# Kernel optimization log

Measured on AMD Instinct MI355X. Metric: run time of the kernel, lower is better.

## Reference

```python
import jax, jax.numpy as jnp
import numpy as np
from jax import lax

MAX_SCALE = 4
SCALES = [2 ** i for i in range(1, MAX_SCALE + 1)]  # [2,4,8,16]
EPS_K = 1e-7        # tf.keras.backend.epsilon()
BN_EPS = 1e-3       # keras BatchNormalization default epsilon


def sample_min_max_scaling(x):
    # per-sample min-max scaling over H, W, C
    mn = jnp.min(x, axis=(1, 2, 3), keepdims=True)
    mx = jnp.max(x, axis=(1, 2, 3), keepdims=True)
    return (x - mn) / (mx - mn + EPS_K)


def box_sum(x, r):
    # depthwise all-ones r x r conv, SAME padding (TF semantics)
    c = x.shape[-1]
    kernel = jnp.ones((r, r, 1, c), dtype=x.dtype)  # HWIO, depthwise
    return lax.conv_general_dilated(
        x, kernel, window_strides=(1, 1), padding='SAME',
        dimension_numbers=('NHWC', 'HWIO', 'NHWC'),
        feature_group_count=c)


def reference(x, gamma, beta, moving_mean, moving_var):
    x = sample_min_max_scaling(x)
    # multi-scale box-filter measures: [B,H,W,C,S]
    measures = jnp.stack([box_sum(x, r) for r in SCALES], axis=-1)
    # OLS slope of log(measure) vs log(scale) across the scale axis
    log_scales = jnp.log(jnp.asarray(SCALES, dtype=x.dtype))       # [S]
    log_measures = jnp.log(measures + EPS_K)                        # [B,H,W,C,S]
    mean_ls = jnp.mean(log_scales)
    mean_lm = jnp.mean(log_measures, axis=-1, keepdims=True)
    dls = log_scales - mean_ls                                      # [S]
    num = jnp.sum((log_measures - mean_lm) * dls, axis=-1)          # [B,H,W,C]
    den = jnp.sum(dls ** 2)
    alphas = num / den
    # BatchNormalization in inference mode (training=False)
    return (alphas - moving_mean) / jnp.sqrt(moving_var + BN_EPS) * gamma + beta


def setup_inputs() -> dict:
    key = jax.random.key(0)
    B, H, W, C = 16, 224, 224, 32
    x = jax.random.normal(key, (B, H, W, C), dtype=jnp.float32)
    return {
        'x': x,
        'gamma': jnp.ones((C,), jnp.float32),
        'beta': jnp.zeros((C,), jnp.float32),
        'moving_mean': jnp.zeros((C,), jnp.float32),
        'moving_var': jnp.ones((C,), jnp.float32),
    }
```

## Files before the change

### kernel.cpp

```cpp
#include <hip/hip_runtime.h>
#include <cstdint>

#define B_ 16
#define H_ 224
#define W_ 224
#define C_ 32
#define TS 32
#define RG 47
#define SR 48
#define SP 49

__device__ __forceinline__ unsigned int enc_f(float f) {
    unsigned int u = __float_as_uint(f);
    return (u & 0x80000000u) ? ~u : (u | 0x80000000u);
}
__device__ __forceinline__ float dec_f(unsigned int u) {
    u = (u & 0x80000000u) ? (u & 0x7FFFFFFFu) : ~u;
    return __uint_as_float(u);
}

__global__ void init_ws(unsigned int* __restrict__ ws) {
    int t = threadIdx.x;
    if (t < 16) ws[t] = 0xFFFFFFFFu;
    else if (t < 32) ws[t] = 0u;
}

__device__ __forceinline__ void blk_minmax(const float* __restrict__ x,
                                           float& mn, float& mx) {
    const int b = blockIdx.x;
    const int chunk = blockIdx.y;
    const int chunkElems = (H_ * W_ * C_) / 64;
    const float4* p = (const float4*)(x + (size_t)b * (H_ * W_ * C_) +
                                      (size_t)chunk * chunkElems);
    const int n4 = chunkElems / 4;
    mn = 3.4e38f; mx = -3.4e38f;
    for (int i = threadIdx.x; i < n4; i += 256) {
        float4 v = p[i];
        mn = fminf(mn, fminf(fminf(v.x, v.y), fminf(v.z, v.w)));
        mx = fmaxf(mx, fmaxf(fmaxf(v.x, v.y), fmaxf(v.z, v.w)));
    }
#pragma unroll
    for (int off = 32; off > 0; off >>= 1) {
        mn = fminf(mn, __shfl_down(mn, off));
        mx = fmaxf(mx, __shfl_down(mx, off));
    }
    __shared__ float smn[4], smx[4];
    const int lane = threadIdx.x & 63, wv = threadIdx.x >> 6;
    if (lane == 0) { smn[wv] = mn; smx[wv] = mx; }
    __syncthreads();
    mn = fminf(fminf(smn[0], smn[1]), fminf(smn[2], smn[3]));
    mx = fmaxf(fmaxf(smx[0], smx[1]), fmaxf(smx[2], smx[3]));
}

__global__ __launch_bounds__(256) void minmax_slots(const float* __restrict__ x,
                                                    float* __restrict__ wsf) {
    float mn, mx;
    blk_minmax(x, mn, mx);
    if (threadIdx.x == 0) {
        wsf[blockIdx.y * 16 + blockIdx.x] = mn;
        wsf[1024 + blockIdx.y * 16 + blockIdx.x] = mx;
    }
}

__global__ __launch_bounds__(256) void minmax_atomic(const float* __restrict__ x,
                                                     unsigned int* __restrict__ ws) {
    float mn, mx;
    blk_minmax(x, mn, mx);
    if (threadIdx.x == 0) {
        atomicMin(&ws[blockIdx.x], enc_f(mn));
        atomicMax(&ws[16 + blockIdx.x], enc_f(mx));
    }
}

template<int CTRL, int MASK>
__device__ __forceinline__ float dpp_add(float x) {
    int t = __builtin_amdgcn_update_dpp(0, (int)__float_as_uint(x),
                                        CTRL, MASK, 0xf, false);
    return x + __uint_as_float((unsigned)t);
}
template<int CTRL, int MASK>
__device__ __forceinline__ void dpp_step4(float4& v) {
    v.x = dpp_add<CTRL, MASK>(v.x);
    v.y = dpp_add<CTRL, MASK>(v.y);
    v.z = dpp_add<CTRL, MASK>(v.z);
    v.w = dpp_add<CTRL, MASK>(v.w);
}
__device__ __forceinline__ void hscan(float4& v) {
    dpp_step4<0x111, 0xf>(v);
    dpp_step4<0x112, 0xf>(v);
    dpp_step4<0x114, 0xf>(v);
    dpp_step4<0x118, 0xf>(v);
    dpp_step4<0x142, 0xa>(v);
    dpp_step4<0x143, 0xc>(v);
}

#define CL(a) (fmaxf((a), 0.0f) + 1e-7f)

#define BOXD(S, o, sc, bx) {                                             \
        float4 q00 = S[hl + (o)][wl + (o)];                              \
        float4 q01 = S[hl + (o)][wl + (o) + (sc)];                       \
        float4 q10 = S[hl + (o) + (sc)][wl + (o)];                       \
        float4 q11 = S[hl + (o) + (sc)][wl + (o) + (sc)];                \
        bx.x = q11.x - q01.x - q10.x + q00.x;                            \
        bx.y = q11.y - q01.y - q10.y + q00.y;                            \
        bx.z = q11.z - q01.z - q10.z + q00.z;                            \
        bx.w = q11.w - q01.w - q10.w + q00.w; }

#define BNPREP(qi, wq, oq) {                                             \
        const int ch0 = chbase + (qi) * 4;                               \
        const float4 g4  = *(const float4*)(gamma + ch0);                \
        const float4 be4 = *(const float4*)(beta  + ch0);                \
        const float4 mm4 = *(const float4*)(mmean + ch0);                \
        const float4 mv4 = *(const float4*)(mvar  + ch0);                \
        float t;                                                         \
        t = g4.x * rsqrtf(mv4.x + 1e-3f);                                \
        wq.x = 0.1f * t; oq.x = be4.x - mm4.x * t;                       \
        t = g4.y * rsqrtf(mv4.y + 1e-3f);                                \
        wq.y = 0.1f * t; oq.y = be4.y - mm4.y * t;                       \
        t = g4.z * rsqrtf(mv4.z + 1e-3f);                                \
        wq.z = 0.1f * t; oq.z = be4.z - mm4.z * t;                       \
        t = g4.w * rsqrtf(mv4.w + 1e-3f);                                \
        wq.w = 0.1f * t; oq.w = be4.w - mm4.w * t; }

#define LSSCOMP(comp, wq, oq, OUT) {                                     \
        const float a2 = CL(b2.comp),  a4 = CL(b4.comp);                 \
        const float a8 = CL(b8.comp),  a16 = CL(b16.comp);               \
        const float Lq = __log2f(a16 * a16 * a16 * a8)                   \
                       - __log2f(a2 * a2 * a2 * a4);                     \
        OUT = fmaf(Lq, wq.comp, oq.comp); }

#define DOQUAD(qi, wq, oq, o4) {                                         \
        const float4 (*S)[SP] = SAT[qi];                                 \
        float4 b2, b4, b8, b16;                                          \
        BOXD(S, 7, 2, b2);                                               \
        BOXD(S, 6, 4, b4);                                               \
        BOXD(S, 4, 8, b8);                                               \
        BOXD(S, 0, 16, b16);                                             \
        LSSCOMP(x, wq, oq, o4.x); LSSCOMP(y, wq, oq, o4.y);              \
        LSSCOMP(z, wq, oq, o4.z); LSSCOMP(w, wq, oq, o4.w); }

template<bool SLOTS>
__global__ __launch_bounds__(512, 4) void lss_kernel(
    const float* __restrict__ x,
    const float* __restrict__ gamma, const float* __restrict__ beta,
    const float* __restrict__ mmean, const float* __restrict__ mvar,
    const unsigned int* __restrict__ ws,
    float* __restrict__ out)
{
    __shared__ float4 SAT[2][SR][SP];

    const int bi = blockIdx.x;
    const int grp = bi >> 5, wi = bi & 31;
    const int tile = grp * 8 + (wi & 7);
    const int s  = (wi >> 3) & 1;
    const int qp = (wi >> 4) & 1;
    const int b = tile / 49;
    const int t2 = tile - b * 49;
    const int th0 = (t2 / 7) * TS;
    const int tw0 = (t2 % 7) * TS;
    const int tid = threadIdx.x;
    const int lane = tid & 63, wv = tid >> 6;
    const int chbase = s * 16 + qp * 8;

    float mn, mx;
    if (SLOTS) {
        const float* wsf = (const float*)ws;
        float vmn = wsf[lane * 16 + b];
        float vmx = wsf[1024 + lane * 16 + b];
#pragma unroll
        for (int off = 32; off > 0; off >>= 1) {
            vmn = fminf(vmn, __shfl_xor(vmn, off));
            vmx = fmaxf(vmx, __shfl_xor(vmx, off));
        }
        mn = vmn; mx = vmx;
    } else {
        mn = dec_f(ws[b]);
        mx = dec_f(ws[16 + b]);
    }
    const float inv = 1.0f / (mx - mn + 1e-7f);
    const float nmi = -mn * inv;

    const float* xb = x + (size_t)b * (H_ * W_ * C_);
    float* ob = out + (size_t)b * (H_ * W_ * C_);

#pragma unroll
    for (int p = 0; p < 6; ++p) {
        const int rr = wv + 8 * p;
        if (rr < RG) {
            const int gh = th0 - 7 + rr;
            const int gw = tw0 - 7 + lane;
            float4 q0 = make_float4(0.f, 0.f, 0.f, 0.f);
            float4 q1 = q0;
            if (lane < RG && gh >= 0 && gh < H_ && gw >= 0 && gw < W_) {
                const float4* p4 = (const float4*)(xb +
                    ((size_t)(gh * W_ + gw)) * C_ + chbase);
                q0 = p4[0]; q1 = p4[1];
                q0.x = fmaf(q0.x, inv, nmi); q0.y = fmaf(q0.y, inv, nmi);
                q0.z = fmaf(q0.z, inv, nmi); q0.w = fmaf(q0.w, inv, nmi);
                q1.x = fmaf(q1.x, inv, nmi); q1.y = fmaf(q1.y, inv, nmi);
                q1.z = fmaf(q1.z, inv, nmi); q1.w = fmaf(q1.w, inv, nmi);
            }
            hscan(q0); hscan(q1);
            if (lane < RG) {
                SAT[0][rr][lane + 1] = q0;
                SAT[1][rr][lane + 1] = q1;
            } else if (lane == 63) {
                const float4 z = make_float4(0.f, 0.f, 0.f, 0.f);
                SAT[0][rr][0] = z; SAT[1][rr][0] = z;
            }
        }
    }
    __syncthreads();

    {
        int q = -1, c = 0;
        if (tid < 192)      { q = 0; c = tid; }
        else if (tid < 384) { q = 1; c = tid - 192; }
        if (q >= 0) {
            float* col = (float*)&SAT[q][0][0] + c;
            float accv = 0.f;
#pragma unroll
            for (int r = 0; r < SR; ++r) {
                const float t = (r < RG) ? col[r * (SP * 4)] : 0.f;
                col[r * (SP * 4)] = accv;
                accv += t;
            }
        }
    }
    __syncthreads();

    {
        const int wl = tid & 31;
        const int hl0 = tid >> 5;
        float4 wq0, oq0, wq1, oq1;
        BNPREP(0, wq0, oq0);
        BNPREP(1, wq1, oq1);
#pragma unroll
        for (int pp = 0; pp < 2; ++pp) {
            const int hl = hl0 + pp * 16;
            float4 o0, o1;
            DOQUAD(0, wq0, oq0, o0);
            DOQUAD(1, wq1, oq1, o1);
            float* dst = ob + ((size_t)((th0 + hl) * W_ + (tw0 + wl))) * C_ + chbase;
            *(float4*)(dst + 0) = o0;
            *(float4*)(dst + 4) = o1;
        }
    }
}

extern "C" void kernel_launch(void* const* d_in, const int* in_sizes, int n_in,
                              void* d_out, int out_size, void* d_ws, size_t ws_size,
                              hipStream_t stream) {
    const float* x     = (const float*)d_in[0];
    const float* gamma = (const float*)d_in[1];
    const float* beta  = (const float*)d_in[2];
    const float* mmean = (const float*)d_in[3];
    const float* mvar  = (const float*)d_in[4];
    float* out = (float*)d_out;
    unsigned int* ws = (unsigned int*)d_ws;

    if (ws_size >= 8192) {
        hipLaunchKernelGGL(minmax_slots, dim3(16, 64), dim3(256), 0, stream,
                           x, (float*)ws);
        hipLaunchKernelGGL((lss_kernel<true>), dim3(98 * 32), dim3(512), 0, stream,
                           x, gamma, beta, mmean, mvar, ws, out);
    } else {
        hipLaunchKernelGGL(init_ws, dim3(1), dim3(64), 0, stream, ws);
        hipLaunchKernelGGL(minmax_atomic, dim3(16, 64), dim3(256), 0, stream, x, ws);
        hipLaunchKernelGGL((lss_kernel<false>), dim3(98 * 32), dim3(512), 0, stream,
                           x, gamma, beta, mmean, mvar, ws, out);
    }
}
```

Measured before the change: 261.7 us.

## Split channel work per block and share row-difference terms across output rows

Each block now handles 4 channels with 256 threads instead of 8 channels with 512 threads, so the block count doubles and shared memory per block halves. In the evaluation phase each thread computes four output rows that are 8 apart and reuses the horizontal SAT differences shared between overlapping boxes, which cuts LDS reads. It also combines the two log2 terms into one per side. The aim is fewer shared-memory reads and higher occupancy. The cost is more registers per thread and 16-byte instead of 32-byte global accesses per pixel.

Measured after the change: 270.3 us. 3.3% more time.

```diff
diff --git a/kernel.cpp b/kernel.cpp
--- a/kernel.cpp
+++ b/kernel.cpp
@@ -94,73 +94,41 @@
     dpp_step4<0x143, 0xc>(v);
 }
 
-#define CL(a) (fmaxf((a), 0.0f) + 1e-7f)
-
-#define BOXD(S, o, sc, bx) {                                             \
-        float4 q00 = S[hl + (o)][wl + (o)];                              \
-        float4 q01 = S[hl + (o)][wl + (o) + (sc)];                       \
-        float4 q10 = S[hl + (o) + (sc)][wl + (o)];                       \
-        float4 q11 = S[hl + (o) + (sc)][wl + (o) + (sc)];                \
-        bx.x = q11.x - q01.x - q10.x + q00.x;                            \
-        bx.y = q11.y - q01.y - q10.y + q00.y;                            \
-        bx.z = q11.z - q01.z - q10.z + q00.z;                            \
-        bx.w = q11.w - q01.w - q10.w + q00.w; }
-
-#define BNPREP(qi, wq, oq) {                                             \
-        const int ch0 = chbase + (qi) * 4;                               \
-        const float4 g4  = *(const float4*)(gamma + ch0);                \
-        const float4 be4 = *(const float4*)(beta  + ch0);                \
-        const float4 mm4 = *(const float4*)(mmean + ch0);                \
-        const float4 mv4 = *(const float4*)(mvar  + ch0);                \
-        float t;                                                         \
-        t = g4.x * rsqrtf(mv4.x + 1e-3f);                                \
-        wq.x = 0.1f * t; oq.x = be4.x - mm4.x * t;                       \
-        t = g4.y * rsqrtf(mv4.y + 1e-3f);                                \
-        wq.y = 0.1f * t; oq.y = be4.y - mm4.y * t;                       \
-        t = g4.z * rsqrtf(mv4.z + 1e-3f);                                \
-        wq.z = 0.1f * t; oq.z = be4.z - mm4.z * t;                       \
-        t = g4.w * rsqrtf(mv4.w + 1e-3f);                                \
-        wq.w = 0.1f * t; oq.w = be4.w - mm4.w * t; }
-
-#define LSSCOMP(comp, wq, oq, OUT) {                                     \
-        const float a2 = CL(b2.comp),  a4 = CL(b4.comp);                 \
-        const float a8 = CL(b8.comp),  a16 = CL(b16.comp);               \
-        const float Lq = __log2f(a16 * a16 * a16 * a8)                   \
-                       - __log2f(a2 * a2 * a2 * a4);                     \
-        OUT = fmaf(Lq, wq.comp, oq.comp); }
-
-#define DOQUAD(qi, wq, oq, o4) {                                         \
-        const float4 (*S)[SP] = SAT[qi];                                 \
-        float4 b2, b4, b8, b16;                                          \
-        BOXD(S, 7, 2, b2);                                               \
-        BOXD(S, 6, 4, b4);                                               \
-        BOXD(S, 4, 8, b8);                                               \
-        BOXD(S, 0, 16, b16);                                             \
-        LSSCOMP(x, wq, oq, o4.x); LSSCOMP(y, wq, oq, o4.y);              \
-        LSSCOMP(z, wq, oq, o4.z); LSSCOMP(w, wq, oq, o4.w); }
+__device__ __forceinline__ float4 f4sub(float4 a, float4 b) {
+    return make_float4(a.x - b.x, a.y - b.y, a.z - b.z, a.w - b.w);
+}
+__device__ __forceinline__ float4 f4mul(float4 a, float4 b) {
+    return make_float4(a.x * b.x, a.y * b.y, a.z * b.z, a.w * b.w);
+}
+__device__ __forceinline__ float4 f4cl(float4 a) {
+    return make_float4(fmaxf(a.x, 0.f) + 1e-7f, fmaxf(a.y, 0.f) + 1e-7f,
+                       fmaxf(a.z, 0.f) + 1e-7f, fmaxf(a.w, 0.f) + 1e-7f);
+}
+__device__ __forceinline__ float4 f4cube(float4 a) {
+    return f4mul(f4mul(a, a), a);
+}
 
 template<bool SLOTS>
-__global__ __launch_bounds__(512, 4) void lss_kernel(
+__global__ __launch_bounds__(256, 4) void lss_kernel(
     const float* __restrict__ x,
     const float* __restrict__ gamma, const float* __restrict__ beta,
     const float* __restrict__ mmean, const float* __restrict__ mvar,
     const unsigned int* __restrict__ ws,
     float* __restrict__ out)
 {
-    __shared__ float4 SAT[2][SR][SP];
+    __shared__ float4 SAT[SR][SP];
 
     const int bi = blockIdx.x;
-    const int grp = bi >> 5, wi = bi & 31;
+    const int grp = bi >> 6, wi = bi & 63;
     const int tile = grp * 8 + (wi & 7);
-    const int s  = (wi >> 3) & 1;
-    const int qp = (wi >> 4) & 1;
+    const int cq = (wi >> 3) & 7;
+    const int chbase = cq * 4;
     const int b = tile / 49;
     const int t2 = tile - b * 49;
     const int th0 = (t2 / 7) * TS;
     const int tw0 = (t2 % 7) * TS;
     const int tid = threadIdx.x;
     const int lane = tid & 63, wv = tid >> 6;
-    const int chbase = s * 16 + qp * 8;
 
     float mn, mx;
     if (SLOTS) {
@@ -184,67 +152,122 @@
     float* ob = out + (size_t)b * (H_ * W_ * C_);
 
 #pragma unroll
-    for (int p = 0; p < 6; ++p) {
-        const int rr = wv + 8 * p;
+    for (int p = 0; p < 12; ++p) {
+        const int rr = wv + 4 * p;
         if (rr < RG) {
             const int gh = th0 - 7 + rr;
             const int gw = tw0 - 7 + lane;
-            float4 q0 = make_float4(0.f, 0.f, 0.f, 0.f);
-            float4 q1 = q0;
+            float4 q = make_float4(0.f, 0.f, 0.f, 0.f);
             if (lane < RG && gh >= 0 && gh < H_ && gw >= 0 && gw < W_) {
-                const float4* p4 = (const float4*)(xb +
-                    ((size_t)(gh * W_ + gw)) * C_ + chbase);
-                q0 = p4[0]; q1 = p4[1];
-                q0.x = fmaf(q0.x, inv, nmi); q0.y = fmaf(q0.y, inv, nmi);
-                q0.z = fmaf(q0.z, inv, nmi); q0.w = fmaf(q0.w, inv, nmi);
-                q1.x = fmaf(q1.x, inv, nmi); q1.y = fmaf(q1.y, inv, nmi);
-                q1.z = fmaf(q1.z, inv, nmi); q1.w = fmaf(q1.w, inv, nmi);
+                q = *(const float4*)(xb + ((size_t)(gh * W_ + gw)) * C_ + chbase);
+                q.x = fmaf(q.x, inv, nmi); q.y = fmaf(q.y, inv, nmi);
+                q.z = fmaf(q.z, inv, nmi); q.w = fmaf(q.w, inv, nmi);
             }
-            hscan(q0); hscan(q1);
-            if (lane < RG) {
-                SAT[0][rr][lane + 1] = q0;
-                SAT[1][rr][lane + 1] = q1;
-            } else if (lane == 63) {
-                const float4 z = make_float4(0.f, 0.f, 0.f, 0.f);
-                SAT[0][rr][0] = z; SAT[1][rr][0] = z;
-            }
+            hscan(q);
+            if (lane < RG) SAT[rr][lane + 1] = q;
+            else if (lane == 63) SAT[rr][0] = make_float4(0.f, 0.f, 0.f, 0.f);
         }
     }
     __syncthreads();
 
+    if (tid < 192) {
+        float* col = (float*)&SAT[0][0] + tid;
+        float accv = 0.f;
+#pragma unroll
+        for (int r = 0; r < SR; ++r) {
+            const float t = (r < RG) ? col[r * (SP * 4)] : 0.f;
+            col[r * (SP * 4)] = accv;
+            accv += t;
+        }
+    }
+    __syncthreads();
+
     {
-        int q = -1, c = 0;
-        if (tid < 192)      { q = 0; c = tid; }
-        else if (tid < 384) { q = 1; c = tid - 192; }
-        if (q >= 0) {
-            float* col = (float*)&SAT[q][0][0] + c;
-            float accv = 0.f;
-#pragma unroll
-            for (int r = 0; r < SR; ++r) {
-                const float t = (r < RG) ? col[r * (SP * 4)] : 0.f;
-                col[r * (SP * 4)] = accv;
-                accv += t;
-            }
-        }
-    }
-    __syncthreads();
-
-    {
+        const int h = tid >> 5;
         const int wl = tid & 31;
-        const int hl0 = tid >> 5;
-        float4 wq0, oq0, wq1, oq1;
-        BNPREP(0, wq0, oq0);
-        BNPREP(1, wq1, oq1);
-#pragma unroll
-        for (int pp = 0; pp < 2; ++pp) {
-            const int hl = hl0 + pp * 16;
-            float4 o0, o1;
-            DOQUAD(0, wq0, oq0, o0);
-            DOQUAD(1, wq1, oq1, o1);
-            float* dst = ob + ((size_t)((th0 + hl) * W_ + (tw0 + wl))) * C_ + chbase;
-            *(float4*)(dst + 0) = o0;
-            *(float4*)(dst + 4) = o1;
-        }
+
+        float4 wq, oq;
+        {
+            const float4 g4  = *(const float4*)(gamma + chbase);
+            const float4 be4 = *(const float4*)(beta  + chbase);
+            const float4 mm4 = *(const float4*)(mmean + chbase);
+            const float4 mv4 = *(const float4*)(mvar  + chbase);
+            float t;
+            t = g4.x * rsqrtf(mv4.x + 1e-3f); wq.x = 0.1f * t; oq.x = be4.x - mm4.x * t;
+            t = g4.y * rsqrtf(mv4.y + 1e-3f); wq.y = 0.1f * t; oq.y = be4.y - mm4.y * t;
+            t = g4.z * rsqrtf(mv4.z + 1e-3f); wq.z = 0.1f * t; oq.z = be4.z - mm4.z * t;
+            t = g4.w * rsqrtf(mv4.w + 1e-3f); wq.w = 0.1f * t; oq.w = be4.w - mm4.w * t;
+        }
+
+        float4 num0, num1, num2, num3;
+        float4 den0, den1, den2, den3;
+
+        {
+            float4 e0 = f4sub(SAT[h     ][wl + 16], SAT[h     ][wl]);
+            float4 e1 = f4sub(SAT[h +  8][wl + 16], SAT[h +  8][wl]);
+            float4 e2 = f4sub(SAT[h + 16][wl + 16], SAT[h + 16][wl]);
+            float4 e3 = f4sub(SAT[h + 24][wl + 16], SAT[h + 24][wl]);
+            float4 e4 = f4sub(SAT[h + 32][wl + 16], SAT[h + 32][wl]);
+            float4 e5 = f4sub(SAT[h + 40][wl + 16], SAT[h + 40][wl]);
+            num0 = f4cube(f4cl(f4sub(e2, e0)));
+            num1 = f4cube(f4cl(f4sub(e3, e1)));
+            num2 = f4cube(f4cl(f4sub(e4, e2)));
+            num3 = f4cube(f4cl(f4sub(e5, e3)));
+        }
+        {
+            float4 e0 = f4sub(SAT[h +  4][wl + 12], SAT[h +  4][wl + 4]);
+            float4 e1 = f4sub(SAT[h + 12][wl + 12], SAT[h + 12][wl + 4]);
+            float4 e2 = f4sub(SAT[h + 20][wl + 12], SAT[h + 20][wl + 4]);
+            float4 e3 = f4sub(SAT[h + 28][wl + 12], SAT[h + 28][wl + 4]);
+            float4 e4 = f4sub(SAT[h + 36][wl + 12], SAT[h + 36][wl + 4]);
+            num0 = f4mul(num0, f4cl(f4sub(e1, e0)));
+            num1 = f4mul(num1, f4cl(f4sub(e2, e1)));
+            num2 = f4mul(num2, f4cl(f4sub(e3, e2)));
+            num3 = f4mul(num3, f4cl(f4sub(e4, e3)));
+        }
+        {
+            float4 t0, b0;
+            t0 = f4sub(SAT[h +  6][wl + 10], SAT[h +  6][wl + 6]);
+            b0 = f4sub(SAT[h + 10][wl + 10], SAT[h + 10][wl + 6]);
+            den0 = f4cl(f4sub(b0, t0));
+            t0 = f4sub(SAT[h + 14][wl + 10], SAT[h + 14][wl + 6]);
+            b0 = f4sub(SAT[h + 18][wl + 10], SAT[h + 18][wl + 6]);
+            den1 = f4cl(f4sub(b0, t0));
+            t0 = f4sub(SAT[h + 22][wl + 10], SAT[h + 22][wl + 6]);
+            b0 = f4sub(SAT[h + 26][wl + 10], SAT[h + 26][wl + 6]);
+            den2 = f4cl(f4sub(b0, t0));
+            t0 = f4sub(SAT[h + 30][wl + 10], SAT[h + 30][wl + 6]);
+            b0 = f4sub(SAT[h + 34][wl + 10], SAT[h + 34][wl + 6]);
+            den3 = f4cl(f4sub(b0, t0));
+        }
+        {
+            float4 t0, b0;
+            t0 = f4sub(SAT[h +  7][wl + 9], SAT[h +  7][wl + 7]);
+            b0 = f4sub(SAT[h +  9][wl + 9], SAT[h +  9][wl + 7]);
+            den0 = f4mul(den0, f4cube(f4cl(f4sub(b0, t0))));
+            t0 = f4sub(SAT[h + 15][wl + 9], SAT[h + 15][wl + 7]);
+            b0 = f4sub(SAT[h + 17][wl + 9], SAT[h + 17][wl + 7]);
+            den1 = f4mul(den1, f4cube(f4cl(f4sub(b0, t0))));
+            t0 = f4sub(SAT[h + 23][wl + 9], SAT[h + 23][wl + 7]);
+            b0 = f4sub(SAT[h + 25][wl + 9], SAT[h + 25][wl + 7]);
+            den2 = f4mul(den2, f4cube(f4cl(f4sub(b0, t0))));
+            t0 = f4sub(SAT[h + 31][wl + 9], SAT[h + 31][wl + 7]);
+            b0 = f4sub(SAT[h + 33][wl + 9], SAT[h + 33][wl + 7]);
+            den3 = f4mul(den3, f4cube(f4cl(f4sub(b0, t0))));
+        }
+#define FIN(NUM, DEN, ROW) {                                             \
+        float4 o4;                                                       \
+        o4.x = fmaf(__log2f(NUM.x) - __log2f(DEN.x), wq.x, oq.x);        \
+        o4.y = fmaf(__log2f(NUM.y) - __log2f(DEN.y), wq.y, oq.y);        \
+        o4.z = fmaf(__log2f(NUM.z) - __log2f(DEN.z), wq.z, oq.z);        \
+        o4.w = fmaf(__log2f(NUM.w) - __log2f(DEN.w), wq.w, oq.w);        \
+        *(float4*)(ob + ((size_t)((th0 + (ROW)) * W_ + (tw0 + wl))) * C_ \
+                   + chbase) = o4; }
+        FIN(num0, den0, h);
+        FIN(num1, den1, h + 8);
+        FIN(num2, den2, h + 16);
+        FIN(num3, den3, h + 24);
+#undef FIN
     }
 }
 
@@ -262,12 +285,12 @@
     if (ws_size >= 8192) {
         hipLaunchKernelGGL(minmax_slots, dim3(16, 64), dim3(256), 0, stream,
                            x, (float*)ws);
-        hipLaunchKernelGGL((lss_kernel<true>), dim3(98 * 32), dim3(512), 0, stream,
+        hipLaunchKernelGGL((lss_kernel<true>), dim3(98 * 64), dim3(256), 0, stream,
                            x, gamma, beta, mmean, mvar, ws, out);
     } else {
         hipLaunchKernelGGL(init_ws, dim3(1), dim3(64), 0, stream, ws);
         hipLaunchKernelGGL(minmax_atomic, dim3(16, 64), dim3(256), 0, stream, x, ws);
-        hipLaunchKernelGGL((lss_kernel<false>), dim3(98 * 32), dim3(512), 0, stream,
+        hipLaunchKernelGGL((lss_kernel<false>), dim3(98 * 64), dim3(256), 0, stream,
                            x, gamma, beta, mmean, mvar, ws, out);
     }
 }
```

## Split channel work to one float4 quad per block to halve LDS and raise occupancy

Applied to the files above, without the earlier changes.

Each block now handles 4 channels instead of 8, so the shared-memory summed-area table shrinks from two float4 planes to one (about 37 KB instead of 75 KB). The grid doubles and launch bounds request 8 blocks per CU instead of 4, aiming for more resident waves to hide memory and LDS latency. In exchange, each block loads its 47x47 halo per 4 channels, so halo reads and the per-tile prologue (min/max reduction, column scan) are duplicated across twice as many blocks. Global accesses become 16-byte per pixel instead of 32-byte, which lowers coalescing efficiency.

Result: no change. 261.7 us (+0.0%).

```diff
diff --git a/kernel.cpp b/kernel.cpp
--- a/kernel.cpp
+++ b/kernel.cpp
@@ -106,22 +106,6 @@
         bx.z = q11.z - q01.z - q10.z + q00.z;                            \
         bx.w = q11.w - q01.w - q10.w + q00.w; }
 
-#define BNPREP(qi, wq, oq) {                                             \
-        const int ch0 = chbase + (qi) * 4;                               \
-        const float4 g4  = *(const float4*)(gamma + ch0);                \
-        const float4 be4 = *(const float4*)(beta  + ch0);                \
-        const float4 mm4 = *(const float4*)(mmean + ch0);                \
-        const float4 mv4 = *(const float4*)(mvar  + ch0);                \
-        float t;                                                         \
-        t = g4.x * rsqrtf(mv4.x + 1e-3f);                                \
-        wq.x = 0.1f * t; oq.x = be4.x - mm4.x * t;                       \
-        t = g4.y * rsqrtf(mv4.y + 1e-3f);                                \
-        wq.y = 0.1f * t; oq.y = be4.y - mm4.y * t;                       \
-        t = g4.z * rsqrtf(mv4.z + 1e-3f);                                \
-        wq.z = 0.1f * t; oq.z = be4.z - mm4.z * t;                       \
-        t = g4.w * rsqrtf(mv4.w + 1e-3f);                                \
-        wq.w = 0.1f * t; oq.w = be4.w - mm4.w * t; }
-
 #define LSSCOMP(comp, wq, oq, OUT) {                                     \
         const float a2 = CL(b2.comp),  a4 = CL(b4.comp);                 \
         const float a8 = CL(b8.comp),  a16 = CL(b16.comp);               \
@@ -129,8 +113,7 @@
                        - __log2f(a2 * a2 * a2 * a4);                     \
         OUT = fmaf(Lq, wq.comp, oq.comp); }
 
-#define DOQUAD(qi, wq, oq, o4) {                                         \
-        const float4 (*S)[SP] = SAT[qi];                                 \
+#define DOQUAD(S, wq, oq, o4) {                                          \
         float4 b2, b4, b8, b16;                                          \
         BOXD(S, 7, 2, b2);                                               \
         BOXD(S, 6, 4, b4);                                               \
@@ -140,27 +123,26 @@
         LSSCOMP(z, wq, oq, o4.z); LSSCOMP(w, wq, oq, o4.w); }
 
 template<bool SLOTS>
-__global__ __launch_bounds__(512, 4) void lss_kernel(
+__global__ __launch_bounds__(512, 8) void lss_kernel(
     const float* __restrict__ x,
     const float* __restrict__ gamma, const float* __restrict__ beta,
     const float* __restrict__ mmean, const float* __restrict__ mvar,
     const unsigned int* __restrict__ ws,
     float* __restrict__ out)
 {
-    __shared__ float4 SAT[2][SR][SP];
+    __shared__ float4 SAT[SR][SP];
 
     const int bi = blockIdx.x;
-    const int grp = bi >> 5, wi = bi & 31;
+    const int grp = bi >> 6, wi = bi & 63;
     const int tile = grp * 8 + (wi & 7);
-    const int s  = (wi >> 3) & 1;
-    const int qp = (wi >> 4) & 1;
+    const int q = (wi >> 3) & 7;
+    const int chbase = q * 4;
     const int b = tile / 49;
     const int t2 = tile - b * 49;
     const int th0 = (t2 / 7) * TS;
     const int tw0 = (t2 % 7) * TS;
     const int tid = threadIdx.x;
     const int lane = tid & 63, wv = tid >> 6;
-    const int chbase = s * 16 + qp * 8;
 
     float mn, mx;
     if (SLOTS) {
@@ -190,41 +172,26 @@
             const int gh = th0 - 7 + rr;
             const int gw = tw0 - 7 + lane;
             float4 q0 = make_float4(0.f, 0.f, 0.f, 0.f);
-            float4 q1 = q0;
             if (lane < RG && gh >= 0 && gh < H_ && gw >= 0 && gw < W_) {
-                const float4* p4 = (const float4*)(xb +
-                    ((size_t)(gh * W_ + gw)) * C_ + chbase);
-                q0 = p4[0]; q1 = p4[1];
+                q0 = *(const float4*)(xb + ((size_t)(gh * W_ + gw)) * C_ + chbase);
                 q0.x = fmaf(q0.x, inv, nmi); q0.y = fmaf(q0.y, inv, nmi);
                 q0.z = fmaf(q0.z, inv, nmi); q0.w = fmaf(q0.w, inv, nmi);
-                q1.x = fmaf(q1.x, inv, nmi); q1.y = fmaf(q1.y, inv, nmi);
-                q1.z = fmaf(q1.z, inv, nmi); q1.w = fmaf(q1.w, inv, nmi);
             }
-            hscan(q0); hscan(q1);
-            if (lane < RG) {
-                SAT[0][rr][lane + 1] = q0;
-                SAT[1][rr][lane + 1] = q1;
-            } else if (lane == 63) {
-                const float4 z = make_float4(0.f, 0.f, 0.f, 0.f);
-                SAT[0][rr][0] = z; SAT[1][rr][0] = z;
-            }
+            hscan(q0);
+            if (lane < RG) SAT[rr][lane + 1] = q0;
+            else if (lane == 63) SAT[rr][0] = make_float4(0.f, 0.f, 0.f, 0.f);
         }
     }
     __syncthreads();
 
-    {
-        int q = -1, c = 0;
-        if (tid < 192)      { q = 0; c = tid; }
-        else if (tid < 384) { q = 1; c = tid - 192; }
-        if (q >= 0) {
-            float* col = (float*)&SAT[q][0][0] + c;
-            float accv = 0.f;
-#pragma unroll
-            for (int r = 0; r < SR; ++r) {
-                const float t = (r < RG) ? col[r * (SP * 4)] : 0.f;
-                col[r * (SP * 4)] = accv;
-                accv += t;
-            }
+    if (tid < 192) {
+        float* col = (float*)&SAT[0][0] + tid;
+        float accv = 0.f;
+#pragma unroll
+        for (int r = 0; r < SR; ++r) {
+            const float t = (r < RG) ? col[r * (SP * 4)] : 0.f;
+            col[r * (SP * 4)] = accv;
+            accv += t;
         }
     }
     __syncthreads();
@@ -232,18 +199,26 @@
     {
         const int wl = tid & 31;
         const int hl0 = tid >> 5;
-        float4 wq0, oq0, wq1, oq1;
-        BNPREP(0, wq0, oq0);
-        BNPREP(1, wq1, oq1);
+
+        float4 wq, oq;
+        {
+            const float4 g4  = *(const float4*)(gamma + chbase);
+            const float4 be4 = *(const float4*)(beta  + chbase);
+            const float4 mm4 = *(const float4*)(mmean + chbase);
+            const float4 mv4 = *(const float4*)(mvar  + chbase);
+            float t;
+            t = g4.x * rsqrtf(mv4.x + 1e-3f); wq.x = 0.1f * t; oq.x = be4.x - mm4.x * t;
+            t = g4.y * rsqrtf(mv4.y + 1e-3f); wq.y = 0.1f * t; oq.y = be4.y - mm4.y * t;
+            t = g4.z * rsqrtf(mv4.z + 1e-3f); wq.z = 0.1f * t; oq.z = be4.z - mm4.z * t;
+            t = g4.w * rsqrtf(mv4.w + 1e-3f); wq.w = 0.1f * t; oq.w = be4.w - mm4.w * t;
+        }
 #pragma unroll
         for (int pp = 0; pp < 2; ++pp) {
             const int hl = hl0 + pp * 16;
-            float4 o0, o1;
-            DOQUAD(0, wq0, oq0, o0);
-            DOQUAD(1, wq1, oq1, o1);
-            float* dst = ob + ((size_t)((th0 + hl) * W_ + (tw0 + wl))) * C_ + chbase;
-            *(float4*)(dst + 0) = o0;
-            *(float4*)(dst + 4) = o1;
+            float4 o4;
+            DOQUAD(SAT, wq, oq, o4);
+            *(float4*)(ob + ((size_t)((th0 + hl) * W_ + (tw0 + wl))) * C_
+                       + chbase) = o4;
         }
     }
 }
@@ -262,12 +237,12 @@
     if (ws_size >= 8192) {
         hipLaunchKernelGGL(minmax_slots, dim3(16, 64), dim3(256), 0, stream,
                            x, (float*)ws);
-        hipLaunchKernelGGL((lss_kernel<true>), dim3(98 * 32), dim3(512), 0, stream,
+        hipLaunchKernelGGL((lss_kernel<true>), dim3(98 * 64), dim3(512), 0, stream,
                            x, gamma, beta, mmean, mvar, ws, out);
     } else {
         hipLaunchKernelGGL(init_ws, dim3(1), dim3(64), 0, stream, ws);
         hipLaunchKernelGGL(minmax_atomic, dim3(16, 64), dim3(256), 0, stream, x, ws);
-        hipLaunchKernelGGL((lss_kernel<false>), dim3(98 * 32), dim3(512), 0, stream,
+        hipLaunchKernelGGL((lss_kernel<false>), dim3(98 * 64), dim3(512), 0, stream,
                            x, gamma, beta, mmean, mvar, ws, out);
     }
 }
```
